# Optimization experiments

Measured on AMD Instinct MI355X. Metric: run time of the kernel, lower is better.

Reference implementation:

```python
import math
import jax, jax.numpy as jnp
import numpy as np

D_MODEL = 1024
NUM_HEADS = 16
HEAD_DIM = D_MODEL // NUM_HEADS
B, T = 4, 2048


def _get_slopes(n_heads: int) -> np.ndarray:
    def pow2_slopes(n):
        start = 2 ** (-(2 ** (-(math.log2(n) - 3))))
        return [start * start ** i for i in range(n)]
    if math.log2(n_heads).is_integer():
        return np.array(pow2_slopes(n_heads), dtype=np.float32)
    closest = 2 ** math.floor(math.log2(n_heads))
    slopes = pow2_slopes(closest)
    slopes += pow2_slopes(2 * closest)[0::2][: n_heads - closest]
    return np.array(slopes[:n_heads], dtype=np.float32)


def setup_inputs() -> dict:
    key = jax.random.key(0)
    ks = jax.random.split(key, 6)
    init = 0.02
    return {
        "x": jax.random.normal(ks[0], (B, T, D_MODEL), dtype=jnp.float32),
        "wq": jax.random.normal(ks[1], (D_MODEL, D_MODEL), dtype=jnp.float32) * init,
        "wk": jax.random.normal(ks[2], (D_MODEL, D_MODEL), dtype=jnp.float32) * init,
        "wv": jax.random.normal(ks[3], (D_MODEL, D_MODEL), dtype=jnp.float32) * init,
        "wo": jax.random.normal(ks[4], (D_MODEL, D_MODEL), dtype=jnp.float32) * init,
        "bo": jnp.zeros((D_MODEL,), dtype=jnp.float32),
    }


def reference(x, wq, wk, wv, wo, bo):
    Bx, Tx, _ = x.shape
    H, Dh = NUM_HEADS, HEAD_DIM
    scale = math.sqrt(Dh)
    # nn.Linear: y = x @ W^T
    q = (x @ wq.T).reshape(Bx, Tx, H, Dh).transpose(0, 2, 1, 3)  # (B,H,T,D)
    k = (x @ wk.T).reshape(Bx, Tx, H, Dh).transpose(0, 2, 1, 3)
    v = (x @ wv.T).reshape(Bx, Tx, H, Dh).transpose(0, 2, 1, 3)
    attn = jnp.einsum("bhqd,bhkd->bhqk", q, k) / scale
    # ALiBi bias: -slope * |i - j|, symmetric distance as in the source
    pos = jnp.arange(Tx)
    dist = -jnp.abs(pos[None, :] - pos[:, None]).astype(jnp.float32)  # (T,T)
    slopes = jnp.asarray(_get_slopes(H))  # (H,)
    attn = attn + slopes[None, :, None, None] * dist[None, None, :, :]
    attn = jax.nn.softmax(attn, axis=-1)
    out = jnp.einsum("bhqk,bhkd->bhqd", attn, v)
    out = out.transpose(0, 2, 1, 3).reshape(Bx, Tx, H * Dh)
    return out @ wo.T + bo
```

## Files before the change

### kernel.cpp

```cpp
#include <hip/hip_runtime.h>

#define DMODEL 1024
#define NHEADS 16
#define HDIM   64
#define BB     4
#define TT     2048

typedef __attribute__((ext_vector_type(8))) short bf16x8;
typedef __attribute__((ext_vector_type(4))) short bf16x4;
typedef __attribute__((ext_vector_type(4))) float f32x4;

#if __has_builtin(__builtin_amdgcn_exp2f)
#define EXP2(x) __builtin_amdgcn_exp2f(x)
#else
#define EXP2(x) __expf(0.69314718f * (x))
#endif

#define C1SCALE 0.18033688f

__device__ inline void async16(const void* g, void* l) {
  __builtin_amdgcn_global_load_lds(
      (const __attribute__((address_space(1))) unsigned int*)g,
      (__attribute__((address_space(3))) unsigned int*)l,
      16, 0, 0);
}

__device__ inline unsigned short f2bf(float x) {
  union { float f; unsigned int u; } c; c.f = x;
  unsigned int r = (c.u + 0x7FFFu + ((c.u >> 16) & 1u)) >> 16;
  return (unsigned short)r;
}

__device__ inline unsigned int pkbf(float x, float y) {
  union { float f; unsigned int u; } a, b; a.f = x; b.f = y;
  return __builtin_amdgcn_perm(b.u, a.u, 0x07060302u);
}

__global__ __launch_bounds__(256) void cvt_all(
    const float* __restrict__ x,  const float* __restrict__ wq,
    const float* __restrict__ wk, const float* __restrict__ wv,
    const float* __restrict__ wo,
    unsigned short* __restrict__ xb, unsigned short* __restrict__ wqkvb,
    unsigned short* __restrict__ wob)
{
  int bid = blockIdx.x;
  const float* src; unsigned short* dst; size_t off;
  if (bid < 8192) { src = x; dst = xb; off = (size_t)bid * 1024; }
  else {
    int w = (bid - 8192) >> 10, r = (bid - 8192) & 1023;
    off = (size_t)r * 1024;
    if (w == 0)      { src = wq; dst = wqkvb; }
    else if (w == 1) { src = wk; dst = wqkvb + 1048576; }
    else if (w == 2) { src = wv; dst = wqkvb + 2097152; }
    else             { src = wo; dst = wob; }
  }
  size_t i = off + threadIdx.x * 4;
  float4 v = *(const float4*)(src + i);
  ushort4 o;
  o.x = f2bf(v.x); o.y = f2bf(v.y); o.z = f2bf(v.z); o.w = f2bf(v.w);
  *(ushort4*)(dst + i) = o;
}

__global__ __launch_bounds__(512, 4) void gemm_qkv(
    const unsigned short* __restrict__ A, const unsigned short* __restrict__ W,
    unsigned short* __restrict__ qw, unsigned short* __restrict__ kw,
    unsigned short* __restrict__ vtw)
{
  __shared__ unsigned short As[2][128 * 64];
  __shared__ unsigned short Bs[2][128 * 64];
  const int tid  = threadIdx.x;
  const int lane = tid & 63;
  const int wave = tid >> 6;
  const int lo   = lane & 15, q4 = lane >> 4;
  const int lo7  = lane & 7;
  const int wm   = wave & 3, wn = wave >> 2;
  const int m0 = blockIdx.x * 128;
  const int nb = blockIdx.y;
  const int n0 = nb * 128;
  const int mid = nb >> 3;

  f32x4 acc[2][4] = {};

  auto stage = [&](int k0, int buf) {
#pragma unroll
    for (int i = 0; i < 2; ++i) {
      int ci = i * 512 + tid;
      int row = ci >> 3;
      int c = (ci & 7) ^ (row & 7);
      async16(A + (size_t)(m0 + row) * DMODEL + k0 + c * 8, (char*)As[buf] + ci * 16);
      async16(W + (size_t)(n0 + row) * DMODEL + k0 + c * 8, (char*)Bs[buf] + ci * 16);
    }
  };

  stage(0, 0);
  for (int it = 0; it < DMODEL / 64; ++it) {
    const int buf = it & 1;
    __syncthreads();
    if (it + 1 < DMODEL / 64) stage((it + 1) * 64, buf ^ 1);
#pragma unroll
    for (int hh = 0; hh < 2; ++hh) {
      bf16x8 af[2], bf[4];
#pragma unroll
      for (int mi = 0; mi < 2; ++mi)
        af[mi] = *(const bf16x8*)&As[buf][(wm * 32 + mi * 16 + lo) * 64 + ((hh * 4 + q4) ^ lo7) * 8];
#pragma unroll
      for (int ni = 0; ni < 4; ++ni)
        bf[ni] = *(const bf16x8*)&Bs[buf][(wn * 64 + ni * 16 + lo) * 64 + ((hh * 4 + q4) ^ lo7) * 8];
#pragma unroll
      for (int mi = 0; mi < 2; ++mi)
#pragma unroll
        for (int ni = 0; ni < 4; ++ni)
          acc[mi][ni] = __builtin_amdgcn_mfma_f32_16x16x32_bf16(af[mi], bf[ni], acc[mi][ni], 0, 0, 0);
    }
  }

  unsigned short* dst = (mid == 0) ? qw : (mid == 1) ? kw : vtw;
  const float sc = (mid == 0) ? C1SCALE : 1.0f;
#pragma unroll
  for (int mi = 0; mi < 2; ++mi) {
#pragma unroll
    for (int ni = 0; ni < 4; ++ni) {
#pragma unroll
      for (int r = 0; r < 4; ++r) {
        int m = m0 + wm * 32 + mi * 16 + q4 * 4 + r;
        int nl = ((nb & 7) * 128) + wn * 64 + ni * 16 + lo;
        float v = acc[mi][ni][r] * sc;
        int b = m >> 11, t = m & (TT - 1);
        int h = nl >> 6, d = nl & 63;
        if (mid == 2)
          dst[(((size_t)(b * NHEADS + h)) * HDIM + d) * TT + t] = f2bf(v);
        else
          dst[(((size_t)(b * NHEADS + h)) * TT + t) * HDIM + d] = f2bf(v);
      }
    }
  }
}

__global__ __launch_bounds__(512, 4) void gemm_out(
    const unsigned short* __restrict__ A, const unsigned short* __restrict__ W,
    const float* __restrict__ bias, float* __restrict__ C)
{
  __shared__ unsigned short As[2][128 * 64];
  __shared__ unsigned short Bs[2][128 * 64];
  const int tid  = threadIdx.x;
  const int lane = tid & 63;
  const int wave = tid >> 6;
  const int lo   = lane & 15, q4 = lane >> 4;
  const int lo7  = lane & 7;
  const int wm   = wave & 3, wn = wave >> 2;
  const int m0 = blockIdx.x * 128, n0 = blockIdx.y * 128;

  f32x4 acc[2][4] = {};

  auto stage = [&](int k0, int buf) {
#pragma unroll
    for (int i = 0; i < 2; ++i) {
      int ci = i * 512 + tid;
      int row = ci >> 3;
      int c = (ci & 7) ^ (row & 7);
      async16(A + (size_t)(m0 + row) * DMODEL + k0 + c * 8, (char*)As[buf] + ci * 16);
      async16(W + (size_t)(n0 + row) * DMODEL + k0 + c * 8, (char*)Bs[buf] + ci * 16);
    }
  };

  stage(0, 0);
  for (int it = 0; it < DMODEL / 64; ++it) {
    const int buf = it & 1;
    __syncthreads();
    if (it + 1 < DMODEL / 64) stage((it + 1) * 64, buf ^ 1);
#pragma unroll
    for (int hh = 0; hh < 2; ++hh) {
      bf16x8 af[2], bf[4];
#pragma unroll
      for (int mi = 0; mi < 2; ++mi)
        af[mi] = *(const bf16x8*)&As[buf][(wm * 32 + mi * 16 + lo) * 64 + ((hh * 4 + q4) ^ lo7) * 8];
#pragma unroll
      for (int ni = 0; ni < 4; ++ni)
        bf[ni] = *(const bf16x8*)&Bs[buf][(wn * 64 + ni * 16 + lo) * 64 + ((hh * 4 + q4) ^ lo7) * 8];
#pragma unroll
      for (int mi = 0; mi < 2; ++mi)
#pragma unroll
        for (int ni = 0; ni < 4; ++ni)
          acc[mi][ni] = __builtin_amdgcn_mfma_f32_16x16x32_bf16(af[mi], bf[ni], acc[mi][ni], 0, 0, 0);
    }
  }

#pragma unroll
  for (int mi = 0; mi < 2; ++mi)
#pragma unroll
    for (int ni = 0; ni < 4; ++ni)
#pragma unroll
      for (int r = 0; r < 4; ++r) {
        int m = m0 + wm * 32 + mi * 16 + q4 * 4 + r;
        int n = n0 + wn * 64 + ni * 16 + lo;
        C[(size_t)m * DMODEL + n] = acc[mi][ni][r] + bias[n];
      }
}

__global__ __launch_bounds__(256, 4) void attn_kernel(
    const unsigned short* __restrict__ Q, const unsigned short* __restrict__ K,
    const unsigned short* __restrict__ Vt, unsigned short* __restrict__ O)
{
  __shared__ unsigned short Ks[2][64 * 64];
  __shared__ unsigned short Vs[2][64 * 64];

  const int tid = threadIdx.x, lane = tid & 63, wave = tid >> 6;
  const int lo = lane & 15, q4 = lane >> 4;
  const int lo7 = lane & 7;
  const int bid = blockIdx.x;
  const int h  = (int)((0x3201765489ABFEDCull >> ((bid >> 6) * 4)) & 15);
  const int qb = bid & 15;
  const int b  = (bid >> 4) & 3;
  const int bh = b * NHEADS + h;
  const float slopeL = exp2f(-0.5f * (float)(h + 1)) * 1.44269504f;
  const int q0 = qb * 128;
  const int wq0 = q0 + wave * 32;

  const int D = (int)(19.407f * exp2f(0.5f * (float)(h + 1)));
  int tlo = q0 - D;
  const int ktlo = (tlo <= 0) ? 0 : (tlo >> 6);
  int thi = (q0 + 127 + D) >> 6;
  const int kthi = (thi > TT / 64 - 1) ? TT / 64 - 1 : thi;

  bf16x8 qf[2][2];
#pragma unroll
  for (int m = 0; m < 2; ++m)
#pragma unroll
    for (int hh = 0; hh < 2; ++hh)
      qf[m][hh] = *(const bf16x8*)(Q + ((size_t)bh * TT + wq0 + m * 16 + lo) * HDIM + hh * 32 + q4 * 8);

  bf16x4 ones4;
  {
    short o = (lo == 0) ? (short)0x3F80 : (short)0;
    ones4 = bf16x4{o, o, o, o};
  }

  f32x4 Oacc[2][4];
  f32x4 lacc[2];
#pragma unroll
  for (int m = 0; m < 2; ++m) {
    lacc[m] = f32x4{0.f, 0.f, 0.f, 0.f};
#pragma unroll
    for (int nd = 0; nd < 4; ++nd) Oacc[m][nd] = f32x4{0.f, 0.f, 0.f, 0.f};
  }

  float eb[2][4];
#pragma unroll
  for (int m = 0; m < 2; ++m)
#pragma unroll
    for (int r = 0; r < 4; ++r)
      eb[m][r] = (float)(wq0 + m * 16 + lo - q4 * 4 - r);

  const unsigned short* kbh = K + (size_t)bh * TT * HDIM;
  const unsigned short* vbh = Vt + (size_t)bh * HDIM * TT;

  auto stage = [&](int kt, int buf) {
#pragma unroll
    for (int i = 0; i < 2; ++i) {
      int ci = i * 256 + tid;
      int row = ci >> 3;
      int c = (ci & 7) ^ (row & 7);
      async16(kbh + (size_t)(kt * 64 + row) * HDIM + c * 8, (char*)Ks[buf] + ci * 16);
      async16(vbh + (size_t)row * TT + kt * 64 + c * 8,     (char*)Vs[buf] + ci * 16);
    }
  };

  stage(ktlo, 0);

  for (int kt = ktlo; kt <= kthi; ++kt) {
    const int buf = (kt - ktlo) & 1;
    __syncthreads();
    if (kt < kthi) stage(kt + 1, buf ^ 1);

    bf16x4 pa[2][4];

#pragma unroll
    for (int ns = 0; ns < 4; ++ns) {
      const int krow = (ns * 16 + lo) * 64;
      bf16x8 kf0 = *(const bf16x8*)&Ks[buf][krow + ((q4) ^ lo7) * 8];
      bf16x8 kf1 = *(const bf16x8*)&Ks[buf][krow + ((4 + q4) ^ lo7) * 8];
      const float kb = (float)(kt * 64 + ns * 16);
#pragma unroll
      for (int m = 0; m < 2; ++m) {
        f32x4 a = {0.f, 0.f, 0.f, 0.f};
        a = __builtin_amdgcn_mfma_f32_16x16x32_bf16(kf0, qf[m][0], a, 0, 0, 0);
        a = __builtin_amdgcn_mfma_f32_16x16x32_bf16(kf1, qf[m][1], a, 0, 0, 0);
        float p[4];
#pragma unroll
        for (int r = 0; r < 4; ++r) {
          float w = eb[m][r] - kb;
          p[r] = EXP2(fmaf(-slopeL, fabsf(w), a[r]));
        }
        union { bf16x4 v; unsigned int u[2]; } pk;
        pk.u[0] = pkbf(p[0], p[1]);
        pk.u[1] = pkbf(p[2], p[3]);
        pa[m][ns] = pk.v;
      }
    }

#pragma unroll
    for (int ns = 0; ns < 4; ++ns) {
#pragma unroll
      for (int nd = 0; nd < 4; ++nd) {
        const int row = nd * 16 + lo;
        const int swc = ((ns * 2 + (q4 >> 1)) ^ (row & 7));
        bf16x4 vb = *(const bf16x4*)&Vs[buf][row * 64 + swc * 8 + (q4 & 1) * 4];
#pragma unroll
        for (int m = 0; m < 2; ++m)
          Oacc[m][nd] = __builtin_amdgcn_mfma_f32_16x16x16bf16_1k(pa[m][ns], vb, Oacc[m][nd], 0, 0, 0);
      }
#pragma unroll
      for (int m = 0; m < 2; ++m)
        lacc[m] = __builtin_amdgcn_mfma_f32_16x16x16bf16_1k(pa[m][ns], ones4, lacc[m], 0, 0, 0);
    }
  }

#pragma unroll
  for (int m = 0; m < 2; ++m)
#pragma unroll
    for (int r = 0; r < 4; ++r) {
      float l = __shfl(lacc[m][r], lane & 48);
      float inv = 1.f / l;
      int t = wq0 + m * 16 + q4 * 4 + r;
#pragma unroll
      for (int nd = 0; nd < 4; ++nd) {
        int d = nd * 16 + lo;
        O[((size_t)(b * TT + t)) * DMODEL + h * HDIM + d] = f2bf(Oacc[m][nd][r] * inv);
      }
    }
}

extern "C" void kernel_launch(void* const* d_in, const int* in_sizes, int n_in,
                              void* d_out, int out_size, void* d_ws, size_t ws_size,
                              hipStream_t stream) {
  const float* x  = (const float*)d_in[0];
  const float* wq = (const float*)d_in[1];
  const float* wk = (const float*)d_in[2];
  const float* wv = (const float*)d_in[3];
  const float* wo = (const float*)d_in[4];
  const float* bo = (const float*)d_in[5];
  float* out = (float*)d_out;

  char* ws = (char*)d_ws;
  const size_t seg  = (size_t)BB * TT * DMODEL * sizeof(unsigned short);
  const size_t wseg = (size_t)DMODEL * DMODEL * sizeof(unsigned short);
  unsigned short* qw    = (unsigned short*)(ws);
  unsigned short* kw    = (unsigned short*)(ws + seg);
  unsigned short* vtw   = (unsigned short*)(ws + 2 * seg);
  unsigned short* ow    = (unsigned short*)(ws + 3 * seg);
  unsigned short* xb    = (unsigned short*)(ws + 4 * seg);
  unsigned short* wqkvb = (unsigned short*)(ws + 5 * seg);
  unsigned short* wob   = (unsigned short*)(ws + 5 * seg + 3 * wseg);

  cvt_all<<<dim3(8192 + 4096), dim3(256), 0, stream>>>(x, wq, wk, wv, wo, xb, wqkvb, wob);

  gemm_qkv<<<dim3(64, 24), dim3(512), 0, stream>>>(xb, wqkvb, qw, kw, vtw);

  attn_kernel<<<dim3(BB * NHEADS * (TT / 128)), dim3(256), 0, stream>>>(qw, kw, vtw, ow);

  gemm_out<<<dim3(64, 8), dim3(512), 0, stream>>>(ow, wob, bo, out);
}
```

Baseline: 246.0 us.

## Use 16x16x32 MFMA for PV via permlane swaps, add setprio around MFMAs

The P·V and row-sum products now use the K=32 bf16 MFMA instead of the K=16 variant. This halves the MFMA instruction count and makes the V LDS reads 16-byte wide. The P fragments from two key sub-tiles are rearranged into the wider operand layout with v_permlane32/16_swap instructions. s_setprio hints are also placed around the MFMA groups so MFMA issue is favoured across waves. The cost is the extra permlane work, and the result depends on the lane-swap layout matching the V swizzle correctly.

```diff
diff --git a/kernel.cpp b/kernel.cpp
--- a/kernel.cpp
+++ b/kernel.cpp
@@ -229,10 +229,10 @@
     for (int hh = 0; hh < 2; ++hh)
       qf[m][hh] = *(const bf16x8*)(Q + ((size_t)bh * TT + wq0 + m * 16 + lo) * HDIM + hh * 32 + q4 * 8);
 
-  bf16x4 ones4;
+  bf16x8 ones8;
   {
     short o = (lo == 0) ? (short)0x3F80 : (short)0;
-    ones4 = bf16x4{o, o, o, o};
+    ones8 = bf16x8{o, o, o, o, o, o, o, o};
   }
 
   f32x4 Oacc[2][4];
@@ -272,46 +272,61 @@
     __syncthreads();
     if (kt < kthi) stage(kt + 1, buf ^ 1);
 
-    bf16x4 pa[2][4];
-
-#pragma unroll
-    for (int ns = 0; ns < 4; ++ns) {
-      const int krow = (ns * 16 + lo) * 64;
-      bf16x8 kf0 = *(const bf16x8*)&Ks[buf][krow + ((q4) ^ lo7) * 8];
-      bf16x8 kf1 = *(const bf16x8*)&Ks[buf][krow + ((4 + q4) ^ lo7) * 8];
-      const float kb = (float)(kt * 64 + ns * 16);
+#pragma unroll
+    for (int pp = 0; pp < 2; ++pp) {
+      unsigned int ua[2][2], ub[2][2];
+#pragma unroll
+      for (int hns = 0; hns < 2; ++hns) {
+        const int ns = pp * 2 + hns;
+        const int krow = (ns * 16 + lo) * 64;
+        bf16x8 kf0 = *(const bf16x8*)&Ks[buf][krow + ((q4) ^ lo7) * 8];
+        bf16x8 kf1 = *(const bf16x8*)&Ks[buf][krow + ((4 + q4) ^ lo7) * 8];
+        const float kb = (float)(kt * 64 + ns * 16);
+#pragma unroll
+        for (int m = 0; m < 2; ++m) {
+          f32x4 a = {0.f, 0.f, 0.f, 0.f};
+          __builtin_amdgcn_s_setprio(1);
+          a = __builtin_amdgcn_mfma_f32_16x16x32_bf16(kf0, qf[m][0], a, 0, 0, 0);
+          a = __builtin_amdgcn_mfma_f32_16x16x32_bf16(kf1, qf[m][1], a, 0, 0, 0);
+          __builtin_amdgcn_s_setprio(0);
+          float pv[4];
+#pragma unroll
+          for (int r = 0; r < 4; ++r) {
+            float w = eb[m][r] - kb;
+            pv[r] = EXP2(fmaf(-slopeL, fabsf(w), a[r]));
+          }
+          ua[hns][m] = pkbf(pv[0], pv[1]);
+          ub[hns][m] = pkbf(pv[2], pv[3]);
+        }
+      }
+
+      bf16x8 paf[2];
 #pragma unroll
       for (int m = 0; m < 2; ++m) {
-        f32x4 a = {0.f, 0.f, 0.f, 0.f};
-        a = __builtin_amdgcn_mfma_f32_16x16x32_bf16(kf0, qf[m][0], a, 0, 0, 0);
-        a = __builtin_amdgcn_mfma_f32_16x16x32_bf16(kf1, qf[m][1], a, 0, 0, 0);
-        float p[4];
-#pragma unroll
-        for (int r = 0; r < 4; ++r) {
-          float w = eb[m][r] - kb;
-          p[r] = EXP2(fmaf(-slopeL, fabsf(w), a[r]));
-        }
-        union { bf16x4 v; unsigned int u[2]; } pk;
-        pk.u[0] = pkbf(p[0], p[1]);
-        pk.u[1] = pkbf(p[2], p[3]);
-        pa[m][ns] = pk.v;
-      }
-    }
-
-#pragma unroll
-    for (int ns = 0; ns < 4; ++ns) {
+        unsigned int w0 = ua[0][m], w2 = ua[1][m];
+        unsigned int w1 = ub[0][m], w3 = ub[1][m];
+        asm("v_permlane32_swap_b32 %0, %1" : "+v"(w0), "+v"(w2));
+        asm("v_permlane16_swap_b32 %0, %1" : "+v"(w0), "+v"(w2));
+        asm("v_permlane32_swap_b32 %0, %1" : "+v"(w1), "+v"(w3));
+        asm("v_permlane16_swap_b32 %0, %1" : "+v"(w1), "+v"(w3));
+        union { bf16x8 v; unsigned int u[4]; } U;
+        U.u[0] = w0; U.u[1] = w1; U.u[2] = w2; U.u[3] = w3;
+        paf[m] = U.v;
+      }
+
 #pragma unroll
       for (int nd = 0; nd < 4; ++nd) {
         const int row = nd * 16 + lo;
-        const int swc = ((ns * 2 + (q4 >> 1)) ^ (row & 7));
-        bf16x4 vb = *(const bf16x4*)&Vs[buf][row * 64 + swc * 8 + (q4 & 1) * 4];
+        bf16x8 vb = *(const bf16x8*)&Vs[buf][row * 64 + ((pp * 4 + q4) ^ lo7) * 8];
+        __builtin_amdgcn_s_setprio(1);
 #pragma unroll
         for (int m = 0; m < 2; ++m)
-          Oacc[m][nd] = __builtin_amdgcn_mfma_f32_16x16x16bf16_1k(pa[m][ns], vb, Oacc[m][nd], 0, 0, 0);
+          Oacc[m][nd] = __builtin_amdgcn_mfma_f32_16x16x32_bf16(paf[m], vb, Oacc[m][nd], 0, 0, 0);
+        __builtin_amdgcn_s_setprio(0);
       }
 #pragma unroll
       for (int m = 0; m < 2; ++m)
-        lacc[m] = __builtin_amdgcn_mfma_f32_16x16x16bf16_1k(pa[m][ns], ones4, lacc[m], 0, 0, 0);
+        lacc[m] = __builtin_amdgcn_mfma_f32_16x16x32_bf16(paf[m], ones8, lacc[m], 0, 0, 0);
     }
   }
 
```

After: 244.1 us. About the same (-0.8%).
